# Kernel tuning notes

Measured on AMD Instinct MI355X. Metric: run time of the kernel, lower is better.

The kernel has to match this reference:

```python
import jax, jax.numpy as jnp
import numpy as np

T, B, C, H = 2048, 8, 512, 8
D = C // H  # head dim = 64


def setup_inputs() -> dict:
    key0 = jax.random.key(0)
    ks = jax.random.split(key0, 12)
    std = 0.02
    inp = {
        "query": jax.random.normal(ks[0], (T, B, C), dtype=jnp.float32),
        "key": jax.random.normal(ks[1], (T, B, C), dtype=jnp.float32),
        "value": jax.random.normal(ks[2], (T, B, C), dtype=jnp.float32),
        "Wq": jax.random.normal(ks[3], (C, C), dtype=jnp.float32) * std,
        "bq": jnp.zeros((C,), dtype=jnp.float32),
        "Wk": jax.random.normal(ks[4], (C, C), dtype=jnp.float32) * std,
        "bk": jnp.zeros((C,), dtype=jnp.float32),
        "Wv": jax.random.normal(ks[5], (C, C), dtype=jnp.float32) * std,
        "bv": jnp.zeros((C,), dtype=jnp.float32),
        "Wo": jax.random.normal(ks[6], (C, C), dtype=jnp.float32) * std,
        "bo": jnp.zeros((C,), dtype=jnp.float32),
    }
    return inp


def reference(query, key, value, Wq, bq, Wk, bk, Wv, bv, Wo, bo):
    # batch_first=False: incoming [T, B, C] -> [B, T, C]
    q_in = jnp.transpose(query, (1, 0, 2))
    k_in = jnp.transpose(key, (1, 0, 2))
    v_in = jnp.transpose(value, (1, 0, 2))

    # nn.Linear: x @ W.T + b, then split heads -> [B, H, T, D]
    def proj(x, W, b):
        y = x @ W.T + b
        return y.reshape(x.shape[0], x.shape[1], H, D).transpose(0, 2, 1, 3)

    q = proj(q_in, Wq, bq)
    k = proj(k_in, Wk, bk)
    v = proj(v_in, Wv, bv)

    # scaled_query_key_softmax: q / sqrt(D), attn_mask=None, dropout p=0 is identity
    scale = 1.0 / jnp.sqrt(jnp.asarray(D, dtype=q.dtype))
    att = jnp.einsum("bhqd,bhkd->bhqk", q * scale, k)
    att = jax.nn.softmax(att, axis=-1)
    y = jnp.einsum("bhqk,bhkd->bhqd", att, v)  # [B, H, T, D]

    # merge heads -> [B, T, C], output projection, back to [T, B, C]
    y = y.transpose(0, 2, 1, 3).reshape(q_in.shape[0], q_in.shape[1], C)
    out = y @ Wo.T + bo
    return jnp.transpose(out, (1, 0, 2))
```

## Files before the change

kernel.cpp:

```cpp
#include <hip/hip_runtime.h>

#define TT 2048
#define BB 8
#define CC 512
#define HH 8
#define DD 64
#define MM (TT*BB)
#define LDP 72
#define QSCALE (0.125f * 1.44269950408889634f)

#define OFF_WQ 0u
#define OFF_WK (512u<<10)
#define OFF_WV (1024u<<10)
#define OFF_WO (1536u<<10)
#define OFF_Q  (2u<<20)
#define OFF_K  (18u<<20)
#define OFF_VT (34u<<20)
#define OFF_V  (50u<<20)
#define OFF_Y  OFF_V

typedef __attribute__((ext_vector_type(8)))  unsigned short us8;
typedef __attribute__((ext_vector_type(4)))  unsigned short us4;
typedef __attribute__((ext_vector_type(4)))  float f4;
typedef __attribute__((ext_vector_type(16))) float f16v;
typedef __attribute__((ext_vector_type(4)))  unsigned int u4;
typedef __bf16 bf8v __attribute__((ext_vector_type(8)));

__device__ __forceinline__ unsigned short f2bf(float f) {
  unsigned u = __float_as_uint(f);
  u += 0x7fffu + ((u >> 16) & 1u);
  return (unsigned short)(u >> 16);
}

__device__ __forceinline__ f4 MFMA(us8 a, us8 b, f4 c) {
  return __builtin_amdgcn_mfma_f32_16x16x32_bf16(
      __builtin_bit_cast(bf8v, a), __builtin_bit_cast(bf8v, b), c, 0, 0, 0);
}

__device__ __forceinline__ f16v MFMA32(us8 a, us8 b, f16v c) {
  return __builtin_amdgcn_mfma_f32_32x32x16_bf16(
      __builtin_bit_cast(bf8v, a), __builtin_bit_cast(bf8v, b), c, 0, 0, 0);
}

__device__ __forceinline__ unsigned cvt_pk_bf16(float lo, float hi) {
  unsigned r;
  asm("v_cvt_pk_bf16_f32 %0, %1, %2" : "=v"(r) : "v"(lo), "v"(hi));
  return r;
}

__global__ __launch_bounds__(256) void prep_w(const float* wq, const float* wk,
                                              const float* wv, const float* wo,
                                              unsigned short* dst) {
  int i = blockIdx.x * 256 + threadIdx.x;
  const float* srcs[4] = {wq, wk, wv, wo};
#pragma unroll
  for (int m = 0; m < 4; m++) {
    f4 v = ((const f4*)srcs[m])[i];
    us4 o;
    o[0] = f2bf(v[0]); o[1] = f2bf(v[1]); o[2] = f2bf(v[2]); o[3] = f2bf(v[3]);
    ((us4*)(dst + m * 262144))[i] = o;
  }
}

template <bool XF32>
__device__ __forceinline__ void gemm_core(const void* Xv, const unsigned short* W,
                                          int m0, int n0, f4 acc[4][4],
                                          unsigned short* XsL, unsigned short* WsL) {
  const int tid = threadIdx.x;
  const int w = tid >> 6, lane = tid & 63, g = lane >> 4, l16 = lane & 15;
  const int wr = w >> 1, wc = w & 1;
#pragma unroll
  for (int m = 0; m < 4; m++)
#pragma unroll
    for (int n = 0; n < 4; n++) acc[m][n] = (f4){0.f, 0.f, 0.f, 0.f};

  for (int kk = 0; kk < CC; kk += 64) {
    __syncthreads();
#pragma unroll
    for (int i = 0; i < 4; i++) {
      int c = tid + 256 * i;
      int r = c >> 3, k8 = c & 7;
      if (XF32) {
        const float* src = (const float*)Xv + (size_t)(m0 + r) * CC + kk + k8 * 8;
        f4 v0 = ((const f4*)src)[0];
        f4 v1 = ((const f4*)src)[1];
        us8 o;
        o[0] = f2bf(v0[0]); o[1] = f2bf(v0[1]); o[2] = f2bf(v0[2]); o[3] = f2bf(v0[3]);
        o[4] = f2bf(v1[0]); o[5] = f2bf(v1[1]); o[6] = f2bf(v1[2]); o[7] = f2bf(v1[3]);
        *(us8*)(&XsL[r * LDP + k8 * 8]) = o;
      } else {
        const unsigned short* src = (const unsigned short*)Xv + (size_t)(m0 + r) * CC + kk + k8 * 8;
        *(us8*)(&XsL[r * LDP + k8 * 8]) = *(const us8*)src;
      }
    }
#pragma unroll
    for (int i = 0; i < 4; i++) {
      int c = tid + 256 * i;
      int r = c >> 3, k8 = c & 7;
      const unsigned short* src = W + (size_t)(n0 + r) * CC + kk + k8 * 8;
      *(us8*)(&WsL[r * LDP + k8 * 8]) = *(const us8*)src;
    }
    __syncthreads();
#pragma unroll
    for (int ks = 0; ks < 2; ks++) {
      us8 a[4], b[4];
#pragma unroll
      for (int m = 0; m < 4; m++)
        a[m] = *(const us8*)(&XsL[(wr * 64 + m * 16 + l16) * LDP + ks * 32 + g * 8]);
#pragma unroll
      for (int n = 0; n < 4; n++)
        b[n] = *(const us8*)(&WsL[(wc * 64 + n * 16 + l16) * LDP + ks * 32 + g * 8]);
#pragma unroll
      for (int m = 0; m < 4; m++)
#pragma unroll
        for (int n = 0; n < 4; n++)
          acc[m][n] = MFMA(a[m], b[n], acc[m][n]);
    }
  }
}

__global__ __launch_bounds__(256) void gemm_qkv(const float* xq, const float* xk, const float* xv,
                                                const float* bq, const float* bk, const float* bv,
                                                char* ws) {
  __shared__ unsigned short XsL[128 * LDP];
  __shared__ unsigned short WsL[128 * LDP];
  const int z = blockIdx.z;
  const float* X    = (z == 0) ? xq : (z == 1) ? xk : xv;
  const float* bias = (z == 0) ? bq : (z == 1) ? bk : bv;
  const unsigned short* W = (const unsigned short*)(ws + (size_t)z * 524288u);
  unsigned short* out = (unsigned short*)(ws + ((z == 0) ? OFF_Q : (z == 1) ? OFF_K : OFF_V));
  const float osc = (z == 0) ? QSCALE : 1.0f;

  const int m0 = blockIdx.x * 128, n0 = blockIdx.y * 128;
  f4 acc[4][4];
  gemm_core<true>(X, W, m0, n0, acc, XsL, WsL);

  const int tid = threadIdx.x, w = tid >> 6, lane = tid & 63, g = lane >> 4, l16 = lane & 15;
  const int wr = w >> 1, wc = w & 1;
#pragma unroll
  for (int n = 0; n < 4; n++) {
    int col = n0 + wc * 64 + n * 16 + l16;
    float bvv = bias[col];
    int h = col >> 6, d = col & 63;
#pragma unroll
    for (int m = 0; m < 4; m++) {
      int rbase = m0 + wr * 64 + m * 16 + 4 * g;
#pragma unroll
      for (int r = 0; r < 4; r++) {
        int row = rbase + r;
        int t = row >> 3, b = row & 7;
        float val = (acc[m][n][r] + bvv) * osc;
        out[(size_t)((b * HH + h) * TT + t) * DD + d] = f2bf(val);
      }
    }
  }
}

__global__ __launch_bounds__(256) void transpose_v(char* ws) {
  __shared__ unsigned short Ts[64 * LDP];
  const unsigned short* V = (const unsigned short*)(ws + OFF_V);
  unsigned short* Vt = (unsigned short*)(ws + OFF_VT);
  const int bh = blockIdx.y, t0 = blockIdx.x * 64;
  const int tid = threadIdx.x;
#pragma unroll
  for (int i = 0; i < 2; i++) {
    int c = tid + 256 * i;
    int r = c >> 3, k8 = c & 7;
    *(us8*)(&Ts[r * LDP + k8 * 8]) =
        *(const us8*)(V + (size_t)(bh * TT + t0 + r) * DD + k8 * 8);
  }
  __syncthreads();
#pragma unroll
  for (int i = 0; i < 2; i++) {
    int c = tid + 256 * i;
    int d = c >> 3, t8 = c & 7;
    us8 o;
#pragma unroll
    for (int j = 0; j < 8; j++) o[j] = Ts[(t8 * 8 + j) * LDP + d];
    *(us8*)(Vt + (size_t)(bh * DD + d) * TT + t0 + t8 * 8) = o;
  }
}

__global__ __launch_bounds__(512) void attn(char* ws) {
  __shared__ unsigned short Ks[64 * 64];
  __shared__ unsigned short Vs[64 * 64];
  __shared__ float Rs[8 * 32];
  const unsigned short* Q  = (const unsigned short*)(ws + OFF_Q);
  const unsigned short* K  = (const unsigned short*)(ws + OFF_K);
  const unsigned short* Vt = (const unsigned short*)(ws + OFF_VT);
  unsigned short* Y = (unsigned short*)(ws + OFF_Y);

  const int bh = blockIdx.y, t0 = blockIdx.x * 256;
  const int tid = threadIdx.x, w = tid >> 6, lane = tid & 63;
  const int l31 = lane & 31, h = lane >> 5;
  const int swz = l31 & 7;

  const unsigned short* Kbh = K + (size_t)bh * TT * DD;
  const unsigned short* Vbh = Vt + (size_t)bh * DD * TT;

  const int qrow = t0 + w * 32 + l31;
  const unsigned short* qp = Q + ((size_t)bh * TT + qrow) * DD + h * 8;
  us8 qf[4];
#pragma unroll
  for (int ks = 0; ks < 4; ks++) qf[ks] = *(const us8*)(qp + ks * 16);

  f16v accy[2];
#pragma unroll
  for (int i = 0; i < 16; i++) { accy[0][i] = 0.f; accy[1][i] = 0.f; }
  float rsum = 0.f;

  const int sr = tid >> 3, sch = tid & 7, schs = sch ^ (sr & 7);
  const unsigned short* Kg = Kbh + (size_t)sr * DD + sch * 8;
  const unsigned short* Vg = Vbh + (size_t)sr * TT + sch * 8;
  char* kdst = (char*)Ks + sr * 128 + schs * 16;
  char* vdst = (char*)Vs + sr * 128 + schs * 16;

  for (int kt = 0; kt < TT; kt += 64) {
    __syncthreads();
    *(us8*)kdst = *(const us8*)(Kg + (size_t)kt * DD);
    *(us8*)vdst = *(const us8*)(Vg + kt);
    __syncthreads();

#pragma unroll
    for (int f = 0; f < 2; f++) {
      f16v s;
#pragma unroll
      for (int i = 0; i < 16; i++) s[i] = 0.f;
#pragma unroll
      for (int ks = 0; ks < 4; ks++) {
        us8 kf = *(const us8*)((char*)Ks + (f * 32 + l31) * 128 + (((ks * 2 + h) ^ swz) * 16));
        s = MFMA32(kf, qf[ks], s);
      }
      float p[16];
#pragma unroll
      for (int r = 0; r < 16; r++) {
        p[r] = __builtin_amdgcn_exp2f(s[r]);
        rsum += p[r];
      }
      unsigned dc0[4], dc1[4];
#pragma unroll
      for (int q2 = 0; q2 < 4; q2++) {
        dc0[q2] = cvt_pk_bf16(p[4 * q2 + 0], p[4 * q2 + 1]);
        dc1[q2] = cvt_pk_bf16(p[4 * q2 + 2], p[4 * q2 + 3]);
      }
#pragma unroll
      for (int kss = 0; kss < 2; kss++) {
        int ks = f * 2 + kss;
        unsigned z0 = h ? dc0[2 * kss + 1] : dc0[2 * kss];
        unsigned y0 = h ? dc0[2 * kss]     : dc0[2 * kss + 1];
        unsigned z1 = h ? dc1[2 * kss + 1] : dc1[2 * kss];
        unsigned y1 = h ? dc1[2 * kss]     : dc1[2 * kss + 1];
        unsigned s0 = __shfl_xor(y0, 32);
        unsigned s1 = __shfl_xor(y1, 32);
        unsigned w0 = h ? s0 : z0;
        unsigned w1 = h ? s1 : z1;
        unsigned w2 = h ? z0 : s0;
        unsigned w3 = h ? z1 : s1;
        u4 av = (u4){w0, w1, w2, w3};
        us8 af = __builtin_bit_cast(us8, av);
#pragma unroll
        for (int nd = 0; nd < 2; nd++) {
          us8 vb = *(const us8*)((char*)Vs + (nd * 32 + l31) * 128 + (((ks * 2 + h) ^ swz) * 16));
          accy[nd] = MFMA32(af, vb, accy[nd]);
        }
      }
    }
  }

  rsum += __shfl_xor(rsum, 32);
  float inv = 1.0f / rsum;
  if (h == 0) Rs[w * 32 + l31] = inv;
  __syncthreads();

  const int b = bh >> 3, hh = bh & 7;
#pragma unroll
  for (int nd = 0; nd < 2; nd++) {
    int d = nd * 32 + l31;
#pragma unroll
    for (int r = 0; r < 16; r++) {
      int q = 8 * (r >> 2) + 4 * h + (r & 3);
      int trow = t0 + w * 32 + q;
      float v = accy[nd][r] * Rs[w * 32 + q];
      Y[(size_t)(b * TT + trow) * CC + hh * DD + d] = f2bf(v);
    }
  }
}

__global__ __launch_bounds__(256) void gemm_oproj(char* ws, const float* bo, float* out) {
  __shared__ unsigned short XsL[128 * LDP];
  __shared__ unsigned short WsL[128 * LDP];
  const unsigned short* X = (const unsigned short*)(ws + OFF_Y);
  const unsigned short* W = (const unsigned short*)(ws + OFF_WO);
  const int m0 = blockIdx.x * 128, n0 = blockIdx.y * 128;
  f4 acc[4][4];
  gemm_core<false>(X, W, m0, n0, acc, XsL, WsL);

  const int tid = threadIdx.x, w = tid >> 6, lane = tid & 63, g = lane >> 4, l16 = lane & 15;
  const int wr = w >> 1, wc = w & 1;
#pragma unroll
  for (int n = 0; n < 4; n++) {
    int col = n0 + wc * 64 + n * 16 + l16;
    float bvv = bo[col];
#pragma unroll
    for (int m = 0; m < 4; m++) {
      int rbase = m0 + wr * 64 + m * 16 + 4 * g;
#pragma unroll
      for (int r = 0; r < 4; r++) {
        int row = rbase + r;
        int b = row >> 11, t = row & 2047;
        out[(size_t)(t * BB + b) * CC + col] = acc[m][n][r] + bvv;
      }
    }
  }
}

extern "C" void kernel_launch(void* const* d_in, const int* in_sizes, int n_in,
                              void* d_out, int out_size, void* d_ws, size_t ws_size,
                              hipStream_t stream) {
  const float* query = (const float*)d_in[0];
  const float* key_  = (const float*)d_in[1];
  const float* value = (const float*)d_in[2];
  const float* Wq = (const float*)d_in[3];
  const float* bq = (const float*)d_in[4];
  const float* Wk = (const float*)d_in[5];
  const float* bk = (const float*)d_in[6];
  const float* Wv = (const float*)d_in[7];
  const float* bv = (const float*)d_in[8];
  const float* Wo = (const float*)d_in[9];
  const float* bo = (const float*)d_in[10];
  char* ws = (char*)d_ws;

  prep_w<<<dim3(256), dim3(256), 0, stream>>>(Wq, Wk, Wv, Wo, (unsigned short*)ws);
  gemm_qkv<<<dim3(128, 4, 3), dim3(256), 0, stream>>>(query, key_, value, bq, bk, bv, ws);
  transpose_v<<<dim3(32, 64), dim3(256), 0, stream>>>(ws);
  attn<<<dim3(8, 64), dim3(512), 0, stream>>>(ws);
  gemm_oproj<<<dim3(128, 4), dim3(256), 0, stream>>>(ws, bo, (float*)d_out);
}
```

Measured before the change: 294.6 us.

## Prefetch GEMM tiles into registers and double KV tile size in attention

Measured after the change: 302.5 us. 1.03x slower.

```diff
diff --git a/kernel.cpp b/kernel.cpp
--- a/kernel.cpp
+++ b/kernel.cpp
@@ -7,6 +7,7 @@
 #define DD 64
 #define MM (TT*BB)
 #define LDP 72
+#define KVB 128
 #define QSCALE (0.125f * 1.44269950408889634f)
 
 #define OFF_WQ 0u
@@ -69,37 +70,52 @@
   const int tid = threadIdx.x;
   const int w = tid >> 6, lane = tid & 63, g = lane >> 4, l16 = lane & 15;
   const int wr = w >> 1, wc = w & 1;
+  const int rr = tid >> 3, k8 = tid & 7;
 #pragma unroll
   for (int m = 0; m < 4; m++)
 #pragma unroll
     for (int n = 0; n < 4; n++) acc[m][n] = (f4){0.f, 0.f, 0.f, 0.f};
 
-  for (int kk = 0; kk < CC; kk += 64) {
-    __syncthreads();
+  f4  xa[4][2];
+  us8 xb[4];
+  us8 wv[4];
+
+  auto LOADT = [&](int kk) {
 #pragma unroll
     for (int i = 0; i < 4; i++) {
-      int c = tid + 256 * i;
-      int r = c >> 3, k8 = c & 7;
+      int r = rr + 32 * i;
       if (XF32) {
         const float* src = (const float*)Xv + (size_t)(m0 + r) * CC + kk + k8 * 8;
-        f4 v0 = ((const f4*)src)[0];
-        f4 v1 = ((const f4*)src)[1];
-        us8 o;
-        o[0] = f2bf(v0[0]); o[1] = f2bf(v0[1]); o[2] = f2bf(v0[2]); o[3] = f2bf(v0[3]);
-        o[4] = f2bf(v1[0]); o[5] = f2bf(v1[1]); o[6] = f2bf(v1[2]); o[7] = f2bf(v1[3]);
-        *(us8*)(&XsL[r * LDP + k8 * 8]) = o;
+        xa[i][0] = ((const f4*)src)[0];
+        xa[i][1] = ((const f4*)src)[1];
       } else {
-        const unsigned short* src = (const unsigned short*)Xv + (size_t)(m0 + r) * CC + kk + k8 * 8;
-        *(us8*)(&XsL[r * LDP + k8 * 8]) = *(const us8*)src;
-      }
-    }
+        xb[i] = *(const us8*)((const unsigned short*)Xv + (size_t)(m0 + r) * CC + kk + k8 * 8);
+      }
+      wv[i] = *(const us8*)(W + (size_t)(n0 + r) * CC + kk + k8 * 8);
+    }
+  };
+  auto WRITET = [&]() {
 #pragma unroll
     for (int i = 0; i < 4; i++) {
-      int c = tid + 256 * i;
-      int r = c >> 3, k8 = c & 7;
-      const unsigned short* src = W + (size_t)(n0 + r) * CC + kk + k8 * 8;
-      *(us8*)(&WsL[r * LDP + k8 * 8]) = *(const us8*)src;
-    }
+      int r = rr + 32 * i;
+      us8 o;
+      if (XF32) {
+        o[0] = f2bf(xa[i][0][0]); o[1] = f2bf(xa[i][0][1]);
+        o[2] = f2bf(xa[i][0][2]); o[3] = f2bf(xa[i][0][3]);
+        o[4] = f2bf(xa[i][1][0]); o[5] = f2bf(xa[i][1][1]);
+        o[6] = f2bf(xa[i][1][2]); o[7] = f2bf(xa[i][1][3]);
+      } else {
+        o = xb[i];
+      }
+      *(us8*)(&XsL[r * LDP + k8 * 8]) = o;
+      *(us8*)(&WsL[r * LDP + k8 * 8]) = wv[i];
+    }
+  };
+
+  LOADT(0);
+  WRITET();
+  for (int t = 0; t < 8; t++) {
+    if (t < 7) LOADT((t + 1) * 64);
     __syncthreads();
 #pragma unroll
     for (int ks = 0; ks < 2; ks++) {
@@ -116,6 +132,8 @@
         for (int n = 0; n < 4; n++)
           acc[m][n] = MFMA(a[m], b[n], acc[m][n]);
     }
+    __syncthreads();
+    if (t < 7) WRITET();
   }
 }
 
@@ -182,8 +200,8 @@
 }
 
 __global__ __launch_bounds__(512) void attn(char* ws) {
-  __shared__ unsigned short Ks[64 * 64];
-  __shared__ unsigned short Vs[64 * 64];
+  __shared__ unsigned short Ks[KVB * 68];
+  __shared__ unsigned short Vs[2][64 * 68];
   __shared__ float Rs[8 * 32];
   const unsigned short* Q  = (const unsigned short*)(ws + OFF_Q);
   const unsigned short* K  = (const unsigned short*)(ws + OFF_K);
@@ -193,7 +211,6 @@
   const int bh = blockIdx.y, t0 = blockIdx.x * 256;
   const int tid = threadIdx.x, w = tid >> 6, lane = tid & 63;
   const int l31 = lane & 31, h = lane >> 5;
-  const int swz = l31 & 7;
 
   const unsigned short* Kbh = K + (size_t)bh * TT * DD;
   const unsigned short* Vbh = Vt + (size_t)bh * DD * TT;
@@ -209,26 +226,40 @@
   for (int i = 0; i < 16; i++) { accy[0][i] = 0.f; accy[1][i] = 0.f; }
   float rsum = 0.f;
 
-  const int sr = tid >> 3, sch = tid & 7, schs = sch ^ (sr & 7);
-  const unsigned short* Kg = Kbh + (size_t)sr * DD + sch * 8;
-  const unsigned short* Vg = Vbh + (size_t)sr * TT + sch * 8;
-  char* kdst = (char*)Ks + sr * 128 + schs * 16;
-  char* vdst = (char*)Vs + sr * 128 + schs * 16;
-
-  for (int kt = 0; kt < TT; kt += 64) {
+  const int sr = tid >> 3, sch = tid & 7;
+  const unsigned short* Kg0 = Kbh + (size_t)sr * DD + sch * 8;
+  const unsigned short* Kg1 = Kbh + (size_t)(64 + sr) * DD + sch * 8;
+  const unsigned short* Vg  = Vbh + (size_t)sr * TT + sch * 8;
+  unsigned short* kd0 = &Ks[sr * 68 + sch * 8];
+  unsigned short* kd1 = &Ks[(64 + sr) * 68 + sch * 8];
+  unsigned short* vd0 = &Vs[0][sr * 68 + sch * 8];
+  unsigned short* vd1 = &Vs[1][sr * 68 + sch * 8];
+
+  us8 kn0 = *(const us8*)Kg0;
+  us8 kn1 = *(const us8*)Kg1;
+  us8 vn0 = *(const us8*)Vg;
+  us8 vn1 = *(const us8*)(Vg + 64);
+
+  for (int kt = 0; kt < TT; kt += KVB) {
     __syncthreads();
-    *(us8*)kdst = *(const us8*)(Kg + (size_t)kt * DD);
-    *(us8*)vdst = *(const us8*)(Vg + kt);
+    *(us8*)kd0 = kn0; *(us8*)kd1 = kn1;
+    *(us8*)vd0 = vn0; *(us8*)vd1 = vn1;
+    if (kt + KVB < TT) {
+      kn0 = *(const us8*)(Kg0 + (size_t)(kt + KVB) * DD);
+      kn1 = *(const us8*)(Kg1 + (size_t)(kt + KVB) * DD);
+      vn0 = *(const us8*)(Vg + kt + KVB);
+      vn1 = *(const us8*)(Vg + kt + KVB + 64);
+    }
     __syncthreads();
 
 #pragma unroll
-    for (int f = 0; f < 2; f++) {
+    for (int f = 0; f < 4; f++) {
       f16v s;
 #pragma unroll
       for (int i = 0; i < 16; i++) s[i] = 0.f;
 #pragma unroll
       for (int ks = 0; ks < 4; ks++) {
-        us8 kf = *(const us8*)((char*)Ks + (f * 32 + l31) * 128 + (((ks * 2 + h) ^ swz) * 16));
+        us8 kf = *(const us8*)(&Ks[(f * 32 + l31) * 68 + (ks * 2 + h) * 8]);
         s = MFMA32(kf, qf[ks], s);
       }
       float p[16];
@@ -260,7 +291,7 @@
         us8 af = __builtin_bit_cast(us8, av);
 #pragma unroll
         for (int nd = 0; nd < 2; nd++) {
-          us8 vb = *(const us8*)((char*)Vs + (nd * 32 + l31) * 128 + (((ks * 2 + h) ^ swz) * 16));
+          us8 vb = *(const us8*)(&Vs[ks >> 2][(nd * 32 + l31) * 68 + ((ks & 3) * 2 + h) * 8]);
           accy[nd] = MFMA32(af, vb, accy[nd]);
         }
       }
```
